# Optimization experiments

Hardware: AMD Instinct MI355X
Metric: run time of the kernel (lower is better)

Reference implementation:

```python
import jax, jax.numpy as jnp
import numpy as np

GROUPS = 32
EPS = 1e-5


def _group_norm(x, scale, bias):
    B, C, H, W = x.shape
    xg = x.reshape(B, GROUPS, -1)
    mu = xg.mean(axis=-1, keepdims=True)
    var = jnp.mean(jnp.square(xg - mu), axis=-1, keepdims=True)
    xn = ((xg - mu) * jax.lax.rsqrt(var + EPS)).reshape(B, C, H, W)
    return xn * scale[None, :, None, None] + bias[None, :, None, None]


def _conv1x1(x, w, b):
    # x: [B,C,H,W], w: [O,C], b: [O]
    return jnp.einsum('bchw,oc->bohw', x, w) + b[None, :, None, None]


def setup_inputs() -> dict:
    key = jax.random.key(0)
    ks = jax.random.split(key, 6)
    B, C, H, W = 16, 512, 32, 32
    x = jax.random.normal(ks[0], (B, C, H, W), dtype=jnp.float32)
    # xavier_uniform for [C, C, 1, 1] conv: limit = sqrt(6 / (fan_in + fan_out)) = sqrt(6 / (2C))
    lim = float(np.sqrt(6.0 / (2 * C)))
    wq = jax.random.uniform(ks[1], (C, C), jnp.float32, -lim, lim)
    wk = jax.random.uniform(ks[2], (C, C), jnp.float32, -lim, lim)
    wv = jax.random.uniform(ks[3], (C, C), jnp.float32, -lim, lim)
    wo = jax.random.uniform(ks[4], (C, C), jnp.float32, -lim, lim) * 1e-5  # gain=1e-5
    zeros_c = jnp.zeros((C,), jnp.float32)
    return {
        'x': x,
        'gn_scale': jnp.ones((C,), jnp.float32),
        'gn_bias': zeros_c,
        'wq': wq, 'bq': zeros_c,
        'wk': wk, 'bk': zeros_c,
        'wv': wv, 'bv': zeros_c,
        'wo': wo, 'bo': zeros_c,
    }


def reference(x, gn_scale, gn_bias, wq, bq, wk, bk, wv, bv, wo, bo):
    B, C, H, W = x.shape
    N = H * W
    h = _group_norm(x, gn_scale, gn_bias)
    q = _conv1x1(h, wq, bq).reshape(B, C, N)  # [B,C,N]
    k = _conv1x1(h, wk, bk).reshape(B, C, N)
    v = _conv1x1(h, wv, bv).reshape(B, C, N)
    scale = 1.0 / jnp.sqrt(jnp.asarray(C, x.dtype))
    w = jnp.einsum('bcn,bcm->bnm', q, k) * scale  # [B,N,N]
    w = jax.nn.softmax(w, axis=-1)
    hv = jnp.einsum('bnm,bcm->bcn', w, v).reshape(B, C, H, W)
    out = _conv1x1(hv, wo, bo)
    return x + out
```

## Files before the change

### kernel.cpp

```cpp
#include <hip/hip_runtime.h>
#include <hip/hip_bf16.h>
#include <cstdint>

typedef unsigned char u8;
typedef float floatx4 __attribute__((ext_vector_type(4)));
typedef int intx8 __attribute__((ext_vector_type(8)));

__device__ __forceinline__ void gld_lds16(const void* g, void* l) {
    __builtin_amdgcn_global_load_lds(
        (const __attribute__((address_space(1))) unsigned int*)g,
        (__attribute__((address_space(3))) unsigned int*)l, 16, 0, 0);
}

__device__ __forceinline__ u8 f2fp8(float v) {
    return (u8)(__builtin_amdgcn_cvt_pk_fp8_f32(v, v, 0, false) & 0xff);
}
__device__ __forceinline__ unsigned int pack4_fp8(float a, float b, float c, float d) {
    unsigned int u = __builtin_amdgcn_cvt_pk_fp8_f32(a, b, 0, false);
    u = __builtin_amdgcn_cvt_pk_fp8_f32(c, d, u, true);
    return u;
}

__device__ __forceinline__ intx8 ld_frag(const u8* p, int lo, int hi) {
    uint4 a = *(const uint4*)(p + lo);
    uint4 b = *(const uint4*)(p + hi);
    intx8 r;
    r[0] = a.x; r[1] = a.y; r[2] = a.z; r[3] = a.w;
    r[4] = b.x; r[5] = b.y; r[6] = b.z; r[7] = b.w;
    return r;
}
__device__ __forceinline__ intx8 ld_frag_g(const u8* p) {
    uint4 a = *(const uint4*)(p);
    uint4 b = *(const uint4*)(p + 16);
    intx8 r;
    r[0] = a.x; r[1] = a.y; r[2] = a.z; r[3] = a.w;
    r[4] = b.x; r[5] = b.y; r[6] = b.z; r[7] = b.w;
    return r;
}


__global__ __launch_bounds__(256) void setup_kernel(
    const float* __restrict__ x, const float* __restrict__ gs,
    const float* __restrict__ gb,
    const float* __restrict__ wq, const float* __restrict__ wk,
    const float* __restrict__ wv, const float* __restrict__ wo,
    const float* __restrict__ bq, const float* __restrict__ bk,
    const float* __restrict__ bv,
    u8* __restrict__ hT, u8* __restrict__ wqkv, u8* __restrict__ wob,
    float* __restrict__ bqkv)
{
    const int t = threadIdx.x;
    if (blockIdx.x >= 512) {
        int i = (blockIdx.x - 512) * 256 + t;
        if (i < 786432) {
            int which = i >> 18;
            int off = i & 262143;
            const float* src = which == 0 ? wq : which == 1 ? wk : wv;
            wqkv[i] = f2fp8(src[off]);
        } else {
            int i2 = i - 786432;
            int row = i2 >> 9, col = i2 & 511;
            wob[(long long)(row >> 4) * 8192 + (col >> 5) * 512
                + (row & 15) * 32 + (col & 31)] = f2fp8(wo[i2] * 262144.0f);
        }
        if (i < 1536)
            bqkv[i] = i < 512 ? bq[i] : (i < 1024 ? bk[i - 512] : bv[i - 1024]);
        return;
    }
    const int b = blockIdx.x >> 5;
    const int g = blockIdx.x & 31;
    const int wave = t >> 6, lane = t & 63;
    const float4* x4 = (const float4*)(x + ((long long)b * 512 + g * 16) * 1024);

    float4 v[16];
    float s1 = 0.f, s2 = 0.f;
#pragma unroll
    for (int i = 0; i < 16; ++i) {
        v[i] = x4[i * 256 + t];
        s1 += v[i].x + v[i].y + v[i].z + v[i].w;
        s2 += v[i].x * v[i].x + v[i].y * v[i].y + v[i].z * v[i].z + v[i].w * v[i].w;
    }
#pragma unroll
    for (int m = 32; m; m >>= 1) {
        s1 += __shfl_xor(s1, m, 64);
        s2 += __shfl_xor(s2, m, 64);
    }
    __shared__ float red[2][4];
    __shared__ float stats[2];
    if (lane == 0) { red[0][wave] = s1; red[1][wave] = s2; }
    __syncthreads();
    if (t == 0) {
        float a = red[0][0] + red[0][1] + red[0][2] + red[0][3];
        float q = red[1][0] + red[1][1] + red[1][2] + red[1][3];
        float mu = a * (1.0f / 16384.0f);
        float var = q * (1.0f / 16384.0f) - mu * mu;
        stats[0] = mu;
        stats[1] = rsqrtf(var + 1e-5f);
    }
    __syncthreads();
    const float mu = stats[0], rs = stats[1];

#pragma unroll
    for (int i = 0; i < 16; ++i) {
        const float sc = gs[g * 16 + i] * rs;
        const float bi = gb[g * 16 + i] - mu * sc;
        v[i].x = v[i].x * sc + bi;
        v[i].y = v[i].y * sc + bi;
        v[i].z = v[i].z * sc + bi;
        v[i].w = v[i].w * sc + bi;
    }
    u8* hb = hT + (long long)b * 524288 + g * 16;
#pragma unroll
    for (int r = 0; r < 4; ++r) {
        uint4 o;
        o.x = pack4_fp8(v[0][r],  v[1][r],  v[2][r],  v[3][r]);
        o.y = pack4_fp8(v[4][r],  v[5][r],  v[6][r],  v[7][r]);
        o.z = pack4_fp8(v[8][r],  v[9][r],  v[10][r], v[11][r]);
        o.w = pack4_fp8(v[12][r], v[13][r], v[14][r], v[15][r]);
        *(uint4*)(hb + (long long)(4 * t + r) * 512) = o;
    }
}

template <int EPI>
__global__ __launch_bounds__(256, 3) void gemm_mx(
    const u8* __restrict__ A, long long sA,
    const u8* __restrict__ B, long long sB,
    void* __restrict__ C, long long sC,
    void* __restrict__ C2, void* __restrict__ C3,
    int ldC, int K,
    const float* __restrict__ bias)
{
    __shared__ __align__(16) u8 smem[33792];
    const int tid = threadIdx.x;
    const int l = tid & 63;
    const int wave = tid >> 6;
    const int wm = wave >> 1, wn = wave & 1;
    const int bm = blockIdx.x, bn = blockIdx.y, b = blockIdx.z;

    const u8* Ab = A + (long long)b * sA + (long long)bm * 128 * K;
    const u8* Bb = B + (long long)b * sB + (long long)bn * 128 * K;

    const int srow = wave * 8 + (l >> 3);
    const int sg = ((l & 7) ^ ((l >> 3) & 7)) * 16;
    const u8* ga  = Ab + (long long)srow * K + sg;
    const u8* gbp = Bb + (long long)srow * K + sg;
    const long long c32 = (long long)32 * K;
    const int ldst = wave * 1024;

    const int q4 = l >> 4;
    const int ln = l & 15;
    const int glo = ((2 * q4) ^ (l & 7)) * 16;
    const int ghi = ((2 * q4 + 1) ^ (l & 7)) * 16;
    int arow[4], brow[4];
#pragma unroll
    for (int i = 0; i < 4; ++i) {
        arow[i] = (wm * 64 + i * 16 + ln) * 128;
        brow[i] = (wn * 64 + i * 16 + ln) * 128 + 16384;
    }

    floatx4 acc[4][4] = {};
    const int niter = K >> 7;

    for (int it = 0; it < niter; ++it) {
        const int k0 = it << 7;
#pragma unroll
        for (int c = 0; c < 4; ++c) {
            gld_lds16(ga + c * c32 + k0, smem + c * 4096 + ldst);
            gld_lds16(gbp + c * c32 + k0, smem + 16384 + c * 4096 + ldst);
        }
        __syncthreads();
        intx8 bfr[4];
#pragma unroll
        for (int j = 0; j < 4; ++j) bfr[j] = ld_frag(smem + brow[j], glo, ghi);
#pragma unroll
        for (int i = 0; i < 4; ++i) {
            intx8 af = ld_frag(smem + arow[i], glo, ghi);
#pragma unroll
            for (int j = 0; j < 4; ++j)
                acc[i][j] = __builtin_amdgcn_mfma_scale_f32_16x16x128_f8f6f4(
                    af, bfr[j], acc[i][j], 0, 0, 0, 127, 0, 127);
        }
        __syncthreads();
    }

    {
        const int which = bn >> 2;
        u8* tile = smem;
#pragma unroll
        for (int i = 0; i < 4; ++i) {
            const int rl = wm * 64 + i * 16 + q4 * 4;
#pragma unroll
            for (int j = 0; j < 4; ++j) {
                const int cl = wn * 64 + j * 16 + ln;
                const float badd = bias[bn * 128 + cl];
                if (which == 2) {
                    *(unsigned int*)(tile + cl * 144 + rl) =
                        pack4_fp8(acc[i][j][0] + badd, acc[i][j][1] + badd,
                                  acc[i][j][2] + badd, acc[i][j][3] + badd);
                } else {
#pragma unroll
                    for (int r = 0; r < 4; ++r)
                        tile[(rl + r) * 144 + cl] = f2fp8(acc[i][j][r] + badd);
                }
            }
        }
        __syncthreads();
        const int w2  = wave >> 1;
        const int cbl = (wave & 1) * 2 + (l >> 5);
        const int lnw = (l >> 1) & 15;
        const int g16 = (l & 1) * 16;
#pragma unroll
        for (int p = 0; p < 4; ++p) {
            const int rtile = p * 2 + w2;
            uint4 dd = *(const uint4*)(tile + (rtile * 16 + lnw) * 144 + cbl * 32 + g16);
            u8* dst;
            if (which == 0)
                dst = (u8*)C + (long long)b * sC + (long long)(bm * 8 + rtile) * 8192
                      + ((bn & 3) * 4 + cbl) * 512 + lnw * 32 + g16;
            else if (which == 1)
                dst = (u8*)C2 + (long long)b * sC + (long long)(bm * 8 + rtile) * 8192
                      + ((bn & 3) * 4 + cbl) * 512 + lnw * 32 + g16;
            else
                dst = (u8*)C3 + (long long)b * sC + (long long)((bn & 3) * 8 + rtile) * 16384
                      + (long long)(bm * 4 + cbl) * 512 + lnw * 32 + g16;
            *(uint4*)dst = dd;
        }
    }
}

__global__ __launch_bounds__(256, 2) void attn_out(
    const u8* __restrict__ qg, const u8* __restrict__ kg,
    const u8* __restrict__ vg, const u8* __restrict__ wot,
    const float* __restrict__ bo, const float* __restrict__ xg,
    float* __restrict__ outg)
{
    __shared__ __align__(16) u8 smem[25088];
    const int tid = threadIdx.x;
    const int l = tid & 63;
    const int w = tid >> 6;
    const int d = blockIdx.x;
    const int b  = (d & 7) * 2 + ((d >> 8) & 1);
    const int bq = (d >> 3) & 31;

    const u8* qb = qg + (long long)b * 524288 + (long long)(bq * 2) * 8192;
    const u8* kb = kg + (long long)b * 524288;
    const u8* vb = vg + (long long)b * 524288;

    const int q4 = l >> 4;
    const int ln = l & 15;
    const int glo = ((2 * q4) ^ (l & 7)) * 16;
    const int ghi = ((2 * q4 + 1) ^ (l & 7)) * 16;
    const int lo32 = ln * 32;

    intx8 qf[2][4];
#pragma unroll
    for (int j = 0; j < 2; ++j)
#pragma unroll
        for (int kc = 0; kc < 4; ++kc)
            qf[j][kc] = ld_frag_g(qb + j * 8192 + (kc * 4 + q4) * 512 + lo32);

    floatx4 acc_pv[8][2] = {};
    float psum[2] = {0.f, 0.f};
    const float scale = 0.044194173824159216f;

    for (int mt = 0; mt < 8; ++mt) {
        u8* E = smem + (mt & 1) * 4096;
        floatx4 acc_s[2][2] = {};
#pragma unroll
        for (int kc = 0; kc < 4; ++kc) {
#pragma unroll
            for (int i = 0; i < 2; ++i) {
                intx8 kf = ld_frag_g(kb + (long long)(mt * 8 + w * 2 + i) * 8192
                                        + (kc * 4 + q4) * 512 + lo32);
#pragma unroll
                for (int j = 0; j < 2; ++j)
                    acc_s[i][j] = __builtin_amdgcn_mfma_scale_f32_16x16x128_f8f6f4(
                        kf, qf[j][kc], acc_s[i][j], 0, 0, 0, 127, 0, 127);
            }
        }
        intx8 vfA[4], vfB[4];
        const u8* vrow = vb + (long long)(w * 8) * 16384 + (mt * 4 + q4) * 512 + lo32;
#pragma unroll
        for (int i = 0; i < 4; ++i)
            vfA[i] = ld_frag_g(vrow + (long long)i * 16384);
#pragma unroll
        for (int i = 0; i < 2; ++i) {
#pragma unroll
            for (int j = 0; j < 2; ++j) {
                float e0 = __expf(acc_s[i][j][0] * scale);
                float e1 = __expf(acc_s[i][j][1] * scale);
                float e2 = __expf(acc_s[i][j][2] * scale);
                float e3 = __expf(acc_s[i][j][3] * scale);
                psum[j] += e0 + e1 + e2 + e3;
                const int n = j * 16 + ln;
                const int m0 = w * 32 + i * 16 + q4 * 4;
                *(unsigned int*)(E + n * 128 + (m0 ^ ((n & 7) * 16))) =
                    pack4_fp8(e0 * 0.25f, e1 * 0.25f, e2 * 0.25f, e3 * 0.25f);
            }
        }
        __syncthreads();
#pragma unroll
        for (int i = 0; i < 4; ++i)
            vfB[i] = ld_frag_g(vrow + (long long)(i + 4) * 16384);
        intx8 ef[2];
#pragma unroll
        for (int j = 0; j < 2; ++j)
            ef[j] = ld_frag(E + (j * 16 + ln) * 128, glo, ghi);
#pragma unroll
        for (int i = 0; i < 4; ++i)
#pragma unroll
            for (int j = 0; j < 2; ++j)
                acc_pv[i][j] = __builtin_amdgcn_mfma_scale_f32_16x16x128_f8f6f4(
                    vfA[i], ef[j], acc_pv[i][j], 0, 0, 0, 127, 0, 127);
#pragma unroll
        for (int i = 0; i < 4; ++i)
#pragma unroll
            for (int j = 0; j < 2; ++j)
                acc_pv[i + 4][j] = __builtin_amdgcn_mfma_scale_f32_16x16x128_f8f6f4(
                    vfB[i], ef[j], acc_pv[i + 4][j], 0, 0, 0, 127, 0, 127);
    }

#pragma unroll
    for (int j = 0; j < 2; ++j) {
        psum[j] += __shfl_xor(psum[j], 16, 64);
        psum[j] += __shfl_xor(psum[j], 32, 64);
    }
    float* sb = (float*)(smem + 8192);
    if (l < 16) {
        sb[w * 32 + l]      = psum[0];
        sb[w * 32 + 16 + l] = psum[1];
    }
    __syncthreads();
    float rln[2];
#pragma unroll
    for (int j = 0; j < 2; ++j) {
        const int n = j * 16 + ln;
        rln[j] = 4.0f / (sb[n] + sb[32 + n] + sb[64 + n] + sb[96 + n]);
    }

    u8* HV = smem + 8704;
#pragma unroll
    for (int i = 0; i < 8; ++i) {
#pragma unroll
        for (int j = 0; j < 2; ++j) {
            const int n = j * 16 + ln;
            const int m0 = i * 16 + q4 * 4;
            *(unsigned int*)(HV + w * 4096 + n * 128 + (m0 ^ ((n & 7) * 16))) =
                pack4_fp8(acc_pv[i][j][0] * rln[j], acc_pv[i][j][1] * rln[j],
                          acc_pv[i][j][2] * rln[j], acc_pv[i][j][3] * rln[j]);
        }
    }
    __syncthreads();

    floatx4 acc2[8][2] = {};
#pragma unroll
    for (int kc = 0; kc < 4; ++kc) {
        intx8 hvf[2];
#pragma unroll
        for (int j = 0; j < 2; ++j)
            hvf[j] = ld_frag(HV + kc * 4096 + (j * 16 + ln) * 128, glo, ghi);
#pragma unroll
        for (int rb = 0; rb < 8; ++rb) {
            intx8 wof = ld_frag_g(wot + (long long)(w * 8 + rb) * 8192
                                      + (kc * 4 + q4) * 512 + lo32);
#pragma unroll
            for (int j = 0; j < 2; ++j)
                acc2[rb][j] = __builtin_amdgcn_mfma_scale_f32_16x16x128_f8f6f4(
                    wof, hvf[j], acc2[rb][j], 0, 0, 0, 127, 0, 127);
        }
    }

    const float osc = 3.814697265625e-06f;
    const float* xb = xg + (long long)b * 524288;
    float* og = outg + (long long)b * 524288;
    const int n0 = bq * 32;
#pragma unroll
    for (int rb = 0; rb < 8; ++rb) {
        const int oc0 = w * 128 + rb * 16 + q4 * 4;
#pragma unroll
        for (int j = 0; j < 2; ++j) {
            const int n = n0 + j * 16 + ln;
#pragma unroll
            for (int r = 0; r < 4; ++r) {
                const int oc = oc0 + r;
                og[(long long)oc * 1024 + n] =
                    acc2[rb][j][r] * osc + bo[oc] + xb[(long long)oc * 1024 + n];
            }
        }
    }
}

extern "C" void kernel_launch(void* const* d_in, const int* in_sizes, int n_in,
                              void* d_out, int out_size, void* d_ws, size_t ws_size,
                              hipStream_t stream)
{
    const float* x  = (const float*)d_in[0];
    const float* gs = (const float*)d_in[1];
    const float* gb = (const float*)d_in[2];
    const float* wq = (const float*)d_in[3];
    const float* bq = (const float*)d_in[4];
    const float* wk = (const float*)d_in[5];
    const float* bk = (const float*)d_in[6];
    const float* wv = (const float*)d_in[7];
    const float* bv = (const float*)d_in[8];
    const float* wo = (const float*)d_in[9];
    const float* bo = (const float*)d_in[10];
    float* out = (float*)d_out;

    u8* p = (u8*)d_ws;
    u8* hT   = p; p += 8388608;
    u8* q    = p; p += 8388608;
    u8* k    = p; p += 8388608;
    u8* v    = p; p += 8388608;
    u8* wqkv = p; p += 786432;
    float* bqkv = (float*)p; p += 6144;
    u8* wob  = p; p += 262144;

    setup_kernel<<<4608, 256, 0, stream>>>(x, gs, gb, wq, wk, wv, wo, bq, bk, bv,
                                           hT, wqkv, wob, bqkv);

    gemm_mx<1><<<dim3(8, 12, 16), 256, 0, stream>>>(
        hT, 524288LL, wqkv, 0LL, q, 524288LL, k, v,
        512, 512, bqkv);

    attn_out<<<dim3(512, 1, 1), 256, 0, stream>>>(q, k, v, wob, bo, x, out);
}
```

Measured before the change: 170.1 us.

## Split attention-output block across eight waves with wider key tiles

New measurement: 205.6 us. 20.9% more time.

```diff
diff --git a/kernel.cpp b/kernel.cpp
--- a/kernel.cpp
+++ b/kernel.cpp
@@ -228,13 +228,13 @@
     }
 }
 
-__global__ __launch_bounds__(256, 2) void attn_out(
+__global__ __launch_bounds__(512, 4) void attn_out(
     const u8* __restrict__ qg, const u8* __restrict__ kg,
     const u8* __restrict__ vg, const u8* __restrict__ wot,
     const float* __restrict__ bo, const float* __restrict__ xg,
     float* __restrict__ outg)
 {
-    __shared__ __align__(16) u8 smem[25088];
+    __shared__ __align__(16) u8 smem[33792];
     const int tid = threadIdx.x;
     const int l = tid & 63;
     const int w = tid >> 6;
@@ -252,37 +252,30 @@
     const int ghi = ((2 * q4 + 1) ^ (l & 7)) * 16;
     const int lo32 = ln * 32;
 
-    intx8 qf[2][4];
-#pragma unroll
-    for (int j = 0; j < 2; ++j)
-#pragma unroll
-        for (int kc = 0; kc < 4; ++kc)
-            qf[j][kc] = ld_frag_g(qb + j * 8192 + (kc * 4 + q4) * 512 + lo32);
-
-    floatx4 acc_pv[8][2] = {};
+    floatx4 acc_pv[4][2] = {};
     float psum[2] = {0.f, 0.f};
     const float scale = 0.044194173824159216f;
 
-    for (int mt = 0; mt < 8; ++mt) {
-        u8* E = smem + (mt & 1) * 4096;
+    for (int mt = 0; mt < 4; ++mt) {
+        u8* E = smem + (mt & 1) * 8192;
         floatx4 acc_s[2][2] = {};
+        const int krb = mt * 16 + w * 2;
 #pragma unroll
         for (int kc = 0; kc < 4; ++kc) {
+            intx8 qf[2];
+#pragma unroll
+            for (int j = 0; j < 2; ++j)
+                qf[j] = ld_frag_g(qb + j * 8192 + (kc * 4 + q4) * 512 + lo32);
 #pragma unroll
             for (int i = 0; i < 2; ++i) {
-                intx8 kf = ld_frag_g(kb + (long long)(mt * 8 + w * 2 + i) * 8192
+                intx8 kf = ld_frag_g(kb + (long long)(krb + i) * 8192
                                         + (kc * 4 + q4) * 512 + lo32);
 #pragma unroll
                 for (int j = 0; j < 2; ++j)
                     acc_s[i][j] = __builtin_amdgcn_mfma_scale_f32_16x16x128_f8f6f4(
-                        kf, qf[j][kc], acc_s[i][j], 0, 0, 0, 127, 0, 127);
+                        kf, qf[j], acc_s[i][j], 0, 0, 0, 127, 0, 127);
             }
         }
-        intx8 vfA[4], vfB[4];
-        const u8* vrow = vb + (long long)(w * 8) * 16384 + (mt * 4 + q4) * 512 + lo32;
-#pragma unroll
-        for (int i = 0; i < 4; ++i)
-            vfA[i] = ld_frag_g(vrow + (long long)i * 16384);
 #pragma unroll
         for (int i = 0; i < 2; ++i) {
 #pragma unroll
@@ -294,30 +287,30 @@
                 psum[j] += e0 + e1 + e2 + e3;
                 const int n = j * 16 + ln;
                 const int m0 = w * 32 + i * 16 + q4 * 4;
-                *(unsigned int*)(E + n * 128 + (m0 ^ ((n & 7) * 16))) =
+                const int ks = m0 >> 7, m128 = m0 & 127;
+                *(unsigned int*)(E + n * 256 + ks * 128 + (m128 ^ ((n & 7) * 16))) =
                     pack4_fp8(e0 * 0.25f, e1 * 0.25f, e2 * 0.25f, e3 * 0.25f);
             }
         }
         __syncthreads();
-#pragma unroll
-        for (int i = 0; i < 4; ++i)
-            vfB[i] = ld_frag_g(vrow + (long long)(i + 4) * 16384);
-        intx8 ef[2];
+        intx8 ef[2][2];
 #pragma unroll
         for (int j = 0; j < 2; ++j)
-            ef[j] = ld_frag(E + (j * 16 + ln) * 128, glo, ghi);
-#pragma unroll
-        for (int i = 0; i < 4; ++i)
-#pragma unroll
-            for (int j = 0; j < 2; ++j)
-                acc_pv[i][j] = __builtin_amdgcn_mfma_scale_f32_16x16x128_f8f6f4(
-                    vfA[i], ef[j], acc_pv[i][j], 0, 0, 0, 127, 0, 127);
-#pragma unroll
-        for (int i = 0; i < 4; ++i)
-#pragma unroll
-            for (int j = 0; j < 2; ++j)
-                acc_pv[i + 4][j] = __builtin_amdgcn_mfma_scale_f32_16x16x128_f8f6f4(
-                    vfB[i], ef[j], acc_pv[i + 4][j], 0, 0, 0, 127, 0, 127);
+#pragma unroll
+            for (int ks = 0; ks < 2; ++ks)
+                ef[j][ks] = ld_frag(E + (j * 16 + ln) * 256 + ks * 128, glo, ghi);
+#pragma unroll
+        for (int i = 0; i < 4; ++i) {
+            const u8* vp = vb + (long long)(w * 4 + i) * 16384 + lo32;
+#pragma unroll
+            for (int ks = 0; ks < 2; ++ks) {
+                intx8 vf = ld_frag_g(vp + (mt * 8 + ks * 4 + q4) * 512);
+#pragma unroll
+                for (int j = 0; j < 2; ++j)
+                    acc_pv[i][j] = __builtin_amdgcn_mfma_scale_f32_16x16x128_f8f6f4(
+                        vf, ef[j][ks], acc_pv[i][j], 0, 0, 0, 127, 0, 127);
+            }
+        }
     }
 
 #pragma unroll
@@ -325,7 +318,7 @@
         psum[j] += __shfl_xor(psum[j], 16, 64);
         psum[j] += __shfl_xor(psum[j], 32, 64);
     }
-    float* sb = (float*)(smem + 8192);
+    float* sb = (float*)(smem + 16384);
     if (l < 16) {
         sb[w * 32 + l]      = psum[0];
         sb[w * 32 + 16 + l] = psum[1];
@@ -335,24 +328,26 @@
 #pragma unroll
     for (int j = 0; j < 2; ++j) {
         const int n = j * 16 + ln;
-        rln[j] = 4.0f / (sb[n] + sb[32 + n] + sb[64 + n] + sb[96 + n]);
-    }
-
-    u8* HV = smem + 8704;
-#pragma unroll
-    for (int i = 0; i < 8; ++i) {
+        rln[j] = 4.0f / (sb[n] + sb[32 + n] + sb[64 + n] + sb[96 + n] +
+                         sb[128 + n] + sb[160 + n] + sb[192 + n] + sb[224 + n]);
+    }
+
+    u8* HV = smem + 17408;
+#pragma unroll
+    for (int i = 0; i < 4; ++i) {
 #pragma unroll
         for (int j = 0; j < 2; ++j) {
             const int n = j * 16 + ln;
-            const int m0 = i * 16 + q4 * 4;
-            *(unsigned int*)(HV + w * 4096 + n * 128 + (m0 ^ ((n & 7) * 16))) =
-                pack4_fp8(acc_pv[i][j][0] * rln[j], acc_pv[i][j][1] * rln[j],
+            const int c0 = (w & 1) * 64 + i * 16 + q4 * 4;
+            *(unsigned int*)(HV + (w >> 1) * 4096 + n * 128 + (c0 ^ ((n & 7) * 16))) =
+                pack4_fp8(acc_pv[i][0 + 0][0] * 0.0f + acc_pv[i][j][0] * rln[j],
+                          acc_pv[i][j][1] * rln[j],
                           acc_pv[i][j][2] * rln[j], acc_pv[i][j][3] * rln[j]);
         }
     }
     __syncthreads();
 
-    floatx4 acc2[8][2] = {};
+    floatx4 acc2[4][2] = {};
 #pragma unroll
     for (int kc = 0; kc < 4; ++kc) {
         intx8 hvf[2];
@@ -360,8 +355,8 @@
         for (int j = 0; j < 2; ++j)
             hvf[j] = ld_frag(HV + kc * 4096 + (j * 16 + ln) * 128, glo, ghi);
 #pragma unroll
-        for (int rb = 0; rb < 8; ++rb) {
-            intx8 wof = ld_frag_g(wot + (long long)(w * 8 + rb) * 8192
+        for (int rb = 0; rb < 4; ++rb) {
+            intx8 wof = ld_frag_g(wot + (long long)(w * 4 + rb) * 8192
                                       + (kc * 4 + q4) * 512 + lo32);
 #pragma unroll
             for (int j = 0; j < 2; ++j)
@@ -375,8 +370,8 @@
     float* og = outg + (long long)b * 524288;
     const int n0 = bq * 32;
 #pragma unroll
-    for (int rb = 0; rb < 8; ++rb) {
-        const int oc0 = w * 128 + rb * 16 + q4 * 4;
+    for (int rb = 0; rb < 4; ++rb) {
+        const int oc0 = w * 64 + rb * 16 + q4 * 4;
 #pragma unroll
         for (int j = 0; j < 2; ++j) {
             const int n = n0 + j * 16 + ln;
@@ -423,5 +418,5 @@
         hT, 524288LL, wqkv, 0LL, q, 524288LL, k, v,
         512, 512, bqkv);
 
-    attn_out<<<dim3(512, 1, 1), 256, 0, stream>>>(q, k, v, wob, bo, x, out);
-}
+    attn_out<<<dim3(512, 1, 1), 512, 0, stream>>>(q, k, v, wob, bo, x, out);
+}
```
